# Kernel optimization log

Hardware: AMD Instinct MI355X
Metric: run time of the kernel (lower is better)

The kernel has to match this reference:

```python
import jax, jax.numpy as jnp
import numpy as np

K_NN = 20
EPS = 1e-5

def _conv1(x, w):
    # 1x1 Conv1d: w [O,C], x [B,C,N] -> [B,O,N]
    return jnp.einsum('oc,bcn->bon', w, x)

def _bn_eval(x, g, b):
    # BatchNorm1d in eval mode with running_mean=0, running_var=1
    return x * (g / np.sqrt(1.0 + EPS))[None, :, None] + b[None, :, None]

def _gn(x, g, b, groups=32):
    B, C, N = x.shape
    xr = x.reshape(B, groups, C // groups, N)
    mu = xr.mean(axis=(2, 3), keepdims=True)
    var = xr.var(axis=(2, 3), keepdims=True)
    xn = ((xr - mu) * jax.lax.rsqrt(var + EPS)).reshape(B, C, N)
    return xn * g[None, :, None] + b[None, :, None]

def _lrelu(x):
    return jnp.where(x >= 0, x, 0.2 * x)

def _graph_cross_attention(x, y, k):
    # x:[B,C,N] query features, y:[B,C,M] key features
    xn = x / jnp.linalg.norm(x, axis=1, keepdims=True)
    yn = y / jnp.linalg.norm(y, axis=1, keepdims=True)
    simi = jnp.einsum('bcn,bcm->bnm', xn, yn)          # cosine similarity [B,N,M]
    s, idx = jax.lax.top_k(simi, k)                    # [B,N,k] values and indices
    yt = jnp.swapaxes(y, 1, 2)                         # [B,M,C]
    nn = jax.vmap(lambda yb, ib: yb[ib])(yt, idx)      # gather neighbors [B,N,k,C]
    xt = jnp.swapaxes(x, 1, 2)                         # [B,N,C]
    diff = nn - xt[:, :, None, :]                      # edge features
    w = jax.nn.softmax(s, axis=-1)                     # attention over k neighbors
    agg = jnp.einsum('bnk,bnkc->bnc', w, diff)         # weighted aggregation
    return jnp.swapaxes(jnp.concatenate([xt, agg], axis=-1), 1, 2)  # [B,2C,N]

def setup_inputs() -> dict:
    key = jax.random.key(0)
    ks = jax.random.split(key, 22)
    B, N = 8, 2048
    f = lambda k, s: jax.random.normal(k, s, dtype=jnp.float32)
    return {
        'x1': f(ks[0], (B, 64, N)),
        'x2': f(ks[1], (B, 64, N)),
        'x3': f(ks[2], (B, 128, N)),
        'y3': f(ks[3], (B, 128, N)),
        'w4': f(ks[4], (256, 256)) * 0.06,
        'bn4_g': 1.0 + 0.1 * f(ks[5], (256,)),
        'bn4_b': 0.1 * f(ks[6], (256,)),
        'w5': f(ks[7], (512, 512)) * 0.04,
        'gn5_g': 1.0 + 0.1 * f(ks[8], (512,)),
        'gn5_b': 0.1 * f(ks[9], (512,)),
        'wm1': f(ks[10], (512, 512)) * 0.04,
        'bm1': 0.02 * f(ks[11], (512,)),
        'gn6_g': 1.0 + 0.1 * f(ks[12], (512,)),
        'gn6_b': 0.1 * f(ks[13], (512,)),
        'wm2': f(ks[14], (256, 512)) * 0.04,
        'bm2': 0.02 * f(ks[15], (256,)),
        'gn7_g': 1.0 + 0.1 * f(ks[16], (256,)),
        'gn7_b': 0.1 * f(ks[17], (256,)),
        'wm3': f(ks[18], (128, 256)) * 0.06,
        'bm3': 0.02 * f(ks[19], (128,)),
        'gn8_g': 1.0 + 0.1 * f(ks[20], (128,)),
        'gn8_b': 0.1 * f(ks[21], (128,)),
    }

def reference(x1, x2, x3, y3, w4, bn4_g, bn4_b, w5, gn5_g, gn5_b, wm1, bm1, gn6_g, gn6_b, wm2, bm2, gn7_g, gn7_b, wm3, bm3, gn8_g, gn8_b):
    x = _graph_cross_attention(x3, y3, K_NN)                  # [B,256,N]
    x4 = _lrelu(_bn_eval(_conv1(x, w4), bn4_g, bn4_b))        # conv4 [B,256,N]
    x = jnp.concatenate([x1, x2, x3, x4], axis=1)             # [B,512,N]
    local_concat = _lrelu(_gn(_conv1(x, w5), gn5_g, gn5_b))   # conv5 [B,512,N]
    gmax = local_concat.max(axis=2)
    gavg = local_concat.mean(axis=2)
    global_vector = jnp.concatenate([gmax, gavg], axis=1)     # [B,1024]
    h = jax.nn.relu(_gn(_conv1(local_concat, wm1) + bm1[None, :, None], gn6_g, gn6_b))
    h = jax.nn.relu(_gn(_conv1(h, wm2) + bm2[None, :, None], gn7_g, gn7_b))
    emb = jax.nn.relu(_gn(_conv1(h, wm3) + bm3[None, :, None], gn8_g, gn8_b))
    return emb, global_vector[:, :, None]
```

## Files before the change

kernel.cpp:

```cpp
#include <hip/hip_runtime.h>
#include <math.h>

#define N2 2048
#define LRELU_S 0.2f
#define BN4_RS 0.9999950000374997f

typedef short bf16x8 __attribute__((ext_vector_type(8)));
typedef float f32x16 __attribute__((ext_vector_type(16)));

__device__ __forceinline__ unsigned short bhi(float v) { return (unsigned short)(__float_as_uint(v) >> 16); }
__device__ __forceinline__ float bhif(float v) { return __uint_as_float(__float_as_uint(v) & 0xFFFF0000u); }
__device__ __forceinline__ float bf2f(unsigned short u) { return __uint_as_float(((unsigned int)u) << 16); }

__device__ __forceinline__ void gl16(const void* g, void* l) {
    __builtin_amdgcn_global_load_lds((const __attribute__((address_space(1))) unsigned int*)g,
                                     (__attribute__((address_space(3))) unsigned int*)l, 16, 0, 0);
}

__device__ __forceinline__ f32x16 z16() {
    f32x16 v;
    #pragma unroll
    for (int i = 0; i < 16; ++i) v[i] = 0.f;
    return v;
}

#define MFMA32 __builtin_amdgcn_mfma_f32_32x32x16_bf16

template<int ASRC, int EPI, int PASSES>
__global__ __launch_bounds__(256) void mgemm(
    const unsigned short* __restrict__ a1H, const unsigned short* __restrict__ a1L, int CA,
    const unsigned short* __restrict__ a2H, const unsigned short* __restrict__ a2L,
    const unsigned short* __restrict__ a3H, const unsigned short* __restrict__ a3L,
    const unsigned short* __restrict__ a4H, const unsigned short* __restrict__ a4L,
    const unsigned short* __restrict__ bH,  const unsigned short* __restrict__ bL, long bBs,
    int Ktot, int OC, int bbase,
    float* __restrict__ outF, unsigned short* __restrict__ oH,
    const float* __restrict__ epg, const float* __restrict__ epb,
    float* __restrict__ cs1, float* __restrict__ cs2)
{
    __shared__ alignas(16) unsigned short lAh[4096], lBh[4096];
    __shared__ alignas(16) unsigned short lAl[PASSES == 3 ? 4096 : 16];
    __shared__ alignas(16) unsigned short lBl[PASSES == 3 ? 4096 : 16];
    const int t  = threadIdx.x;
    const int n0 = blockIdx.x * 128;
    const int o0 = blockIdx.y * 128;
    const int bz = blockIdx.z;
    const int b  = bbase + bz;

    const int lane = t & 63;
    const int h    = lane >> 5;
    const int l31  = lane & 31;
    const int wid  = t >> 6;
    const int wm   = wid >> 1;
    const int wn   = wid & 1;
    const int sw   = (l31 >> 1) & 3;

    f32x16 acc00 = z16(), acc01 = z16(), acc10 = z16(), acc11 = z16();

    const int q0 = t, q1 = t + 256;
    const int r0 = q0 >> 2, p0 = q0 & 3, c0s = p0 ^ ((r0 >> 1) & 3);
    const int r1 = q1 >> 2, p1 = q1 & 3, c1s = p1 ^ ((r1 >> 1) & 3);

    const int rA0 = (wm * 64 + l31) * 32, rA1 = rA0 + 1024;
    const int rB0 = (wn * 64 + l31) * 32, rB1 = rB0 + 1024;

    for (int kc = 0; kc < Ktot; kc += 32) {
        const unsigned short *sAH, *sAL; int koff, Cs;
        if (ASRC == 0)      { sAH = a1H; sAL = a1L; koff = kc;       Cs = CA; }
        else if (ASRC == 1) {
            if (kc < 128)   { sAH = a1H; sAL = a1L; koff = kc;       Cs = 128; }
            else            { sAH = a2H; sAL = a2L; koff = kc - 128; Cs = 128; }
        } else {
            if (kc < 64)        { sAH = a1H; sAL = a1L; koff = kc;       Cs = 64;  }
            else if (kc < 128)  { sAH = a2H; sAL = a2L; koff = kc - 64;  Cs = 64;  }
            else if (kc < 256)  { sAH = a3H; sAL = a3L; koff = kc - 128; Cs = 128; }
            else                { sAH = a4H; sAL = a4L; koff = kc - 256; Cs = 256; }
        }
        __syncthreads();
        {
            long ga = ((long)b * N2 + n0 + r0) * Cs + koff + c0s * 8;
            long gb = (long)b * bBs + (long)(o0 + r0) * Ktot + kc + c0s * 8;
            gl16(sAH + ga, lAh + q0 * 8);
            gl16(bH + gb, lBh + q0 * 8);
            if (PASSES == 3) { gl16(sAL + ga, lAl + q0 * 8); gl16(bL + gb, lBl + q0 * 8); }
            long ga1 = ((long)b * N2 + n0 + r1) * Cs + koff + c1s * 8;
            long gb1 = (long)b * bBs + (long)(o0 + r1) * Ktot + kc + c1s * 8;
            gl16(sAH + ga1, lAh + q1 * 8);
            gl16(bH + gb1, lBh + q1 * 8);
            if (PASSES == 3) { gl16(sAL + ga1, lAl + q1 * 8); gl16(bL + gb1, lBl + q1 * 8); }
        }
        __syncthreads();
        #pragma unroll
        for (int s = 0; s < 2; ++s) {
            const int off = ((s * 2 + h) ^ sw) * 8;
            bf16x8 a0h = *(const bf16x8*)(lAh + rA0 + off);
            bf16x8 a1h_ = *(const bf16x8*)(lAh + rA1 + off);
            bf16x8 b0h = *(const bf16x8*)(lBh + rB0 + off);
            bf16x8 b1h = *(const bf16x8*)(lBh + rB1 + off);
            acc00 = MFMA32(a0h, b0h, acc00, 0, 0, 0);
            acc01 = MFMA32(a0h, b1h, acc01, 0, 0, 0);
            acc10 = MFMA32(a1h_, b0h, acc10, 0, 0, 0);
            acc11 = MFMA32(a1h_, b1h, acc11, 0, 0, 0);
            if (PASSES == 3) {
                bf16x8 a0l = *(const bf16x8*)(lAl + rA0 + off);
                bf16x8 a1l_ = *(const bf16x8*)(lAl + rA1 + off);
                bf16x8 b0l = *(const bf16x8*)(lBl + rB0 + off);
                bf16x8 b1l = *(const bf16x8*)(lBl + rB1 + off);
                acc00 = MFMA32(a0h, b0l, acc00, 0, 0, 0);
                acc00 = MFMA32(a0l, b0h, acc00, 0, 0, 0);
                acc01 = MFMA32(a0h, b1l, acc01, 0, 0, 0);
                acc01 = MFMA32(a0l, b1h, acc01, 0, 0, 0);
                acc10 = MFMA32(a1h_, b0l, acc10, 0, 0, 0);
                acc10 = MFMA32(a1l_, b0h, acc10, 0, 0, 0);
                acc11 = MFMA32(a1h_, b1l, acc11, 0, 0, 0);
                acc11 = MFMA32(a1l_, b1h, acc11, 0, 0, 0);
            }
        }
    }

    #pragma unroll
    for (int ni = 0; ni < 2; ++ni) {
        const int o = o0 + wn * 64 + ni * 32 + l31;
        float sc = 0.f, sh = 0.f, bias = 0.f;
        if (EPI == 1) { sc = epg[o] * BN4_RS; sh = epb[o]; }
        if (EPI == 2) { bias = epb ? epb[o] : 0.f; }
        float s1 = 0.f, s2 = 0.f;
        #pragma unroll
        for (int mi = 0; mi < 2; ++mi) {
            #pragma unroll
            for (int r = 0; r < 16; ++r) {
                const int n = n0 + wm * 64 + mi * 32 + (r & 3) + 8 * (r >> 2) + 4 * h;
                float v = (ni == 0) ? (mi == 0 ? acc00[r] : acc10[r])
                                    : (mi == 0 ? acc01[r] : acc11[r]);
                const long oi = ((long)bz * N2 + n) * (long)OC + o;
                if (EPI == 0) {
                    outF[oi] = v;
                } else if (EPI == 1) {
                    v = fmaf(v, sc, sh);
                    v = v >= 0.f ? v : LRELU_S * v;
                    oH[oi] = bhi(v);
                } else {
                    v += bias;
                    outF[oi] = v;
                    s1 += v; s2 = fmaf(v, v, s2);
                }
            }
        }
        if (EPI == 2) {
            s1 += __shfl_xor(s1, 32);
            s2 += __shfl_xor(s2, 32);
            if (h == 0) {
                atomicAdd(cs1 + bz * OC + o, s1);
                atomicAdd(cs2 + bz * OC + o, s2);
            }
        }
    }
}

__global__ void normK(const float* __restrict__ x3, const float* __restrict__ y3,
                      float* __restrict__ invnx, float* __restrict__ invny)
{
    const int n = blockIdx.x * 256 + threadIdx.x;
    const int b = blockIdx.y;
    const float* src = blockIdx.z ? y3 : x3;
    float ss = 0.f;
    for (int c = 0; c < 128; ++c) {
        float v = src[((long)b * 128 + c) * N2 + n];
        ss = fmaf(v, v, ss);
    }
    (blockIdx.z ? invny : invnx)[b * N2 + n] = rsqrtf(ss);
}

template<int MODE>
__global__ __launch_bounds__(256) void tsplitK(
    const float* __restrict__ in, int C,
    unsigned short* __restrict__ tHi, const float* __restrict__ invn,
    unsigned short* __restrict__ sHi, unsigned short* __restrict__ sLo,
    float* __restrict__ tF)
{
    __shared__ float lt[64 * 65];
    const int t = threadIdx.x;
    const int n0 = blockIdx.x * 64, c0 = blockIdx.y * 64, b = blockIdx.z;
    {
        const int nl = t & 63;
        const int cb = t >> 6;
        #pragma unroll
        for (int i = 0; i < 16; ++i) {
            const int cl = cb + 4 * i;
            lt[nl * 65 + cl] = in[((long)b * C + c0 + cl) * N2 + n0 + nl];
        }
    }
    __syncthreads();
    const int cl = t & 63;
    const int nb = t >> 6;
    #pragma unroll
    for (int i = 0; i < 16; ++i) {
        const int nl = nb + 4 * i;
        const float v = lt[nl * 65 + cl];
        const long oi = ((long)b * N2 + n0 + nl) * C + c0 + cl;
        if (MODE & 1) tHi[oi] = bhi(v);
        if (MODE & 2) {
            const float svv = v * invn[b * N2 + n0 + nl];
            sHi[oi] = bhi(svv); sLo[oi] = bhi(svv - bhif(svv));
        }
        if (MODE & 4) tF[oi] = v;
    }
}

__global__ void wsplitK(const float* __restrict__ w4, const float* __restrict__ w5,
    const float* __restrict__ wm1, const float* __restrict__ wm2, const float* __restrict__ wm3,
    unsigned short* __restrict__ w4h, unsigned short* __restrict__ w5h,
    unsigned short* __restrict__ m1h, unsigned short* __restrict__ m2h,
    unsigned short* __restrict__ m3h)
{
    const int y = blockIdx.y;
    const int idx = blockIdx.x * 256 + threadIdx.x;
    float v; unsigned short* dh;
    if (y == 0) {
        if (idx >= 256 * 256) return;
        const int k = idx & 255;
        v = w4[idx];
        if (k < 128) v -= w4[idx + 128];
        dh = w4h;
    } else if (y == 1) {
        if (idx >= 512 * 512) return;
        v = w5[idx]; dh = w5h;
    } else if (y == 2) {
        if (idx >= 512 * 512) return;
        v = wm1[idx]; dh = m1h;
    } else if (y == 3) {
        if (idx >= 256 * 512) return;
        v = wm2[idx]; dh = m2h;
    } else {
        if (idx >= 128 * 256) return;
        v = wm3[idx]; dh = m3h;
    }
    dh[idx] = bhi(v);
}

__global__ __launch_bounds__(256) void topkK(const float* __restrict__ simi,
    float* __restrict__ topw, int* __restrict__ topi, int bbase)
{
    __shared__ unsigned int hist[256];
    __shared__ unsigned int bcast[2];
    __shared__ unsigned int cnt[2];
    __shared__ float selv[20];
    __shared__ int   seli[20];
    const int t  = threadIdx.x;
    const int n  = blockIdx.x;
    const int bl = blockIdx.y;
    const float* row = simi + ((long)bl * N2 + n) * N2;

    float    f[8];
    unsigned u[8];
    {
        const float4 v0 = *(const float4*)(row + 4 * t);
        const float4 v1 = *(const float4*)(row + 1024 + 4 * t);
        f[0] = v0.x; f[1] = v0.y; f[2] = v0.z; f[3] = v0.w;
        f[4] = v1.x; f[5] = v1.y; f[6] = v1.z; f[7] = v1.w;
        #pragma unroll
        for (int i = 0; i < 8; ++i) {
            unsigned ub = __float_as_uint(f[i]);
            u[i] = ub ^ (((int)ub >> 31) | 0x80000000u);
        }
    }

    unsigned prefix = 0;
    unsigned kneed  = 20;
    #pragma unroll
    for (int pass = 0; pass < 4; ++pass) {
        const int shift = 24 - 8 * pass;
        const unsigned pmask = (pass == 0) ? 0u : (0xFFFFFFFFu << (shift + 8));
        hist[t] = 0;
        __syncthreads();
        #pragma unroll
        for (int i = 0; i < 8; ++i)
            if ((u[i] & pmask) == prefix)
                atomicAdd(&hist[(u[i] >> shift) & 255], 1u);
        __syncthreads();
        if (t < 64) {
            const unsigned h0 = hist[4 * t], h1 = hist[4 * t + 1];
            const unsigned h2 = hist[4 * t + 2], h3 = hist[4 * t + 3];
            const unsigned s3 = h3, s2 = h2 + s3, s1 = h1 + s2, s0 = h0 + s1;
            unsigned inc = s0;
            #pragma unroll
            for (int off = 1; off < 64; off <<= 1) {
                const unsigned o = __shfl_down(inc, off);
                if (t + off < 64) inc += o;
            }
            const unsigned excl = inc - s0;
            const unsigned sf[5] = {excl + s0, excl + s1, excl + s2, excl + s3, excl};
            #pragma unroll
            for (int j = 0; j < 4; ++j) {
                if (sf[j] >= kneed && sf[j + 1] < kneed) {
                    bcast[0] = 4 * t + j;
                    bcast[1] = kneed - sf[j + 1];
                }
            }
        }
        __syncthreads();
        prefix |= bcast[0] << shift;
        kneed   = bcast[1];
        __syncthreads();
    }

    if (t == 0) { cnt[0] = 0; cnt[1] = 0; }
    __syncthreads();
    const unsigned Tu = prefix;
    const int eqneed = (int)kneed;
    const int gt     = 20 - eqneed;
    #pragma unroll
    for (int i = 0; i < 8; ++i) {
        const int idx = (i < 4) ? (4 * t + i) : (1024 + 4 * t + (i - 4));
        if (u[i] > Tu) {
            const unsigned s = atomicAdd(&cnt[0], 1u);
            selv[s] = f[i]; seli[s] = idx;
        } else if (u[i] == Tu) {
            const unsigned e = atomicAdd(&cnt[1], 1u);
            if ((int)e < eqneed) { selv[gt + e] = f[i]; seli[gt + e] = idx; }
        }
    }
    __syncthreads();

    if (t < 64) {
        const float v = (t < 20) ? selv[t] : -1e30f;
        float m = v;
        #pragma unroll
        for (int off = 1; off < 32; off <<= 1) m = fmaxf(m, __shfl_xor(m, off, 32));
        const float e = (t < 20) ? expf(v - m) : 0.f;
        float s = e;
        #pragma unroll
        for (int off = 1; off < 32; off <<= 1) s += __shfl_xor(s, off, 32);
        if (t < 20) {
            const long base = (((long)(bbase + bl)) * N2 + n) * 20;
            topw[base + t] = e / s;
            topi[base + t] = seli[t];
        }
    }
}

__global__ __launch_bounds__(256) void aggK(const float* __restrict__ yT,
    const float* __restrict__ topw, const int* __restrict__ topi,
    unsigned short* __restrict__ Gh)
{
    const int t  = threadIdx.x;
    const int c4 = (t & 31) * 4;
    const int ns = t >> 5;
    const int b  = blockIdx.x;
    const int n  = blockIdx.y * 8 + ns;
    const long tb = ((long)b * N2 + n) * 20;
    const float* yb = yT + (long)b * N2 * 128 + c4;

    float a0 = 0.f, a1 = 0.f, a2 = 0.f, a3 = 0.f;
    #pragma unroll
    for (int k = 0; k < 20; ++k) {
        const float w  = topw[tb + k];
        const int  idx = topi[tb + k];
        const float4 v = *(const float4*)(yb + (long)idx * 128);
        a0 = fmaf(w, v.x, a0);
        a1 = fmaf(w, v.y, a1);
        a2 = fmaf(w, v.z, a2);
        a3 = fmaf(w, v.w, a3);
    }
    const long oi = ((long)b * N2 + n) * 128 + c4;
    ushort4 hh;
    hh.x = bhi(a0); hh.y = bhi(a1); hh.z = bhi(a2); hh.w = bhi(a3);
    *(ushort4*)(Gh + oi) = hh;
}

__global__ void statsK(const float* __restrict__ cs1, const float* __restrict__ cs2,
    float* __restrict__ stats, int C)
{
    const int t = threadIdx.x;
    const int b = t >> 5, g = t & 31;
    const int cpg = C >> 5;
    float s1 = 0.f, s2 = 0.f;
    for (int j = 0; j < cpg; ++j) {
        s1 += cs1[b * C + g * cpg + j];
        s2 += cs2[b * C + g * cpg + j];
    }
    const float cnt = (float)(cpg * N2);
    const float mu = s1 / cnt;
    const float var = s2 / cnt - mu * mu;
    stats[t * 2] = mu;
    stats[t * 2 + 1] = rsqrtf(var + 1e-5f);
}

template<int ACT, int LC>
__global__ void gnapplyK(const float* __restrict__ pre, const float* __restrict__ stats,
    const float* __restrict__ gamma, const float* __restrict__ beta,
    unsigned short* __restrict__ oH)
{
    const long i4 = ((long)blockIdx.x * 256 + threadIdx.x) * 4;
    const int C = 1 << LC;
    const int c = (int)(i4 & (C - 1));
    const int bn = (int)(i4 >> LC);
    const int b = bn >> 11;
    const int g = c >> (LC - 5);
    const float mu = stats[(b * 32 + g) * 2];
    const float rs = stats[(b * 32 + g) * 2 + 1];
    const float4 gm = *(const float4*)(gamma + c);
    const float4 bt = *(const float4*)(beta + c);
    const float4 v = *(const float4*)(pre + i4);
    const float vals[4] = {v.x, v.y, v.z, v.w};
    const float gms[4] = {gm.x, gm.y, gm.z, gm.w};
    const float bts[4] = {bt.x, bt.y, bt.z, bt.w};
    unsigned short hs[4];
    #pragma unroll
    for (int j = 0; j < 4; ++j) {
        float x = (vals[j] - mu) * (rs * gms[j]) + bts[j];
        x = (ACT == 0) ? (x >= 0.f ? x : LRELU_S * x) : (x >= 0.f ? x : 0.f);
        hs[j] = bhi(x);
    }
    ushort4 hh; hh.x = hs[0]; hh.y = hs[1]; hh.z = hs[2]; hh.w = hs[3];
    *(ushort4*)(oH + i4) = hh;
}

__global__ __launch_bounds__(256) void gnfinalK(const float* __restrict__ pre,
    const float* __restrict__ stats, const float* __restrict__ gamma,
    const float* __restrict__ beta, float* __restrict__ out)
{
    __shared__ float lt[64 * 65];
    const int t = threadIdx.x;
    const int n0 = blockIdx.x * 64, c0 = blockIdx.y * 64, b = blockIdx.z;
    {
        const int cl = t & 63;
        const int nb = t >> 6;
        const int c = c0 + cl;
        const int g = c >> 2;
        const float mu = stats[(b * 32 + g) * 2];
        const float rs = stats[(b * 32 + g) * 2 + 1];
        const float sc = rs * gamma[c], sh = beta[c] - mu * sc;
        #pragma unroll
        for (int i = 0; i < 16; ++i) {
            const int nl = nb + 4 * i;
            float v = pre[((long)b * N2 + n0 + nl) * 128 + c];
            v = v * sc + sh;
            lt[cl * 65 + nl] = v > 0.f ? v : 0.f;
        }
    }
    __syncthreads();
    const int nl = t & 63;
    const int cb = t >> 6;
    #pragma unroll
    for (int i = 0; i < 16; ++i) {
        const int cl = cb + 4 * i;
        out[((long)b * 128 + c0 + cl) * N2 + n0 + nl] = lt[cl * 65 + nl];
    }
}

__global__ __launch_bounds__(256) void pool1K(const unsigned short* __restrict__ lcH,
    float* __restrict__ pmax, float* __restrict__ psum)
{
    __shared__ float lmx[512], lsm[512];
    const int t  = threadIdx.x;
    const int cq = t & 127;
    const int rp = t >> 7;
    const int nch = blockIdx.x;
    const int b   = blockIdx.y;
    float mx[4] = {-1e30f, -1e30f, -1e30f, -1e30f};
    float sm[4] = {0.f, 0.f, 0.f, 0.f};
    for (int i = 0; i < 32; ++i) {
        const int n = nch * 64 + 2 * i + rp;
        const long base = ((long)b * N2 + n) * 512 + cq * 4;
        const ushort4 hh = *(const ushort4*)(lcH + base);
        const float v0 = bf2f(hh.x);
        const float v1 = bf2f(hh.y);
        const float v2 = bf2f(hh.z);
        const float v3 = bf2f(hh.w);
        mx[0] = fmaxf(mx[0], v0); sm[0] += v0;
        mx[1] = fmaxf(mx[1], v1); sm[1] += v1;
        mx[2] = fmaxf(mx[2], v2); sm[2] += v2;
        mx[3] = fmaxf(mx[3], v3); sm[3] += v3;
    }
    if (rp) {
        #pragma unroll
        for (int j = 0; j < 4; ++j) { lmx[cq * 4 + j] = mx[j]; lsm[cq * 4 + j] = sm[j]; }
    }
    __syncthreads();
    if (!rp) {
        const long pb = ((long)(b * 32 + nch)) * 512 + cq * 4;
        #pragma unroll
        for (int j = 0; j < 4; ++j) {
            pmax[pb + j] = fmaxf(mx[j], lmx[cq * 4 + j]);
            psum[pb + j] = sm[j] + lsm[cq * 4 + j];
        }
    }
}

__global__ void pool2K(const float* __restrict__ pmax, const float* __restrict__ psum,
                       float* __restrict__ gv)
{
    const int t = threadIdx.x;
    const int b = blockIdx.x;
    float mx0 = -1e30f, mx1 = -1e30f, s0 = 0.f, s1 = 0.f;
    for (int nch = 0; nch < 32; ++nch) {
        const long pb = ((long)(b * 32 + nch)) * 512 + 2 * t;
        const float2 pm = *(const float2*)(pmax + pb);
        const float2 ps = *(const float2*)(psum + pb);
        mx0 = fmaxf(mx0, pm.x); mx1 = fmaxf(mx1, pm.y);
        s0 += ps.x; s1 += ps.y;
    }
    gv[b * 1024 + 2 * t]           = mx0;
    gv[b * 1024 + 2 * t + 1]       = mx1;
    gv[b * 1024 + 512 + 2 * t]     = s0 * (1.f / 2048.f);
    gv[b * 1024 + 512 + 2 * t + 1] = s1 * (1.f / 2048.f);
}

extern "C" void kernel_launch(void* const* d_in, const int* in_sizes, int n_in,
                              void* d_out, int out_size, void* d_ws, size_t ws_size,
                              hipStream_t stream)
{
    const float* x1    = (const float*)d_in[0];
    const float* x2    = (const float*)d_in[1];
    const float* x3    = (const float*)d_in[2];
    const float* y3    = (const float*)d_in[3];
    const float* w4    = (const float*)d_in[4];
    const float* bn4g  = (const float*)d_in[5];
    const float* bn4b  = (const float*)d_in[6];
    const float* w5    = (const float*)d_in[7];
    const float* gn5g  = (const float*)d_in[8];
    const float* gn5b  = (const float*)d_in[9];
    const float* wm1   = (const float*)d_in[10];
    const float* bm1   = (const float*)d_in[11];
    const float* gn6g  = (const float*)d_in[12];
    const float* gn6b  = (const float*)d_in[13];
    const float* wm2   = (const float*)d_in[14];
    const float* bm2   = (const float*)d_in[15];
    const float* gn7g  = (const float*)d_in[16];
    const float* gn7b  = (const float*)d_in[17];
    const float* wm3   = (const float*)d_in[18];
    const float* bm3   = (const float*)d_in[19];
    const float* gn8g  = (const float*)d_in[20];
    const float* gn8b  = (const float*)d_in[21];
    float* out = (float*)d_out;
    (void)in_sizes; (void)n_in; (void)out_size; (void)ws_size;

    char* ws = (char*)d_ws;
    float*          simiF = (float*)(ws + 0);
    float*          bufPS = (float*)(ws + 0);
    unsigned short* lcH   = (unsigned short*)(ws + 134217728);
    unsigned short* h1H   = (unsigned short*)(ws + 150994944);
    unsigned short* x4H   = (unsigned short*)(ws + 167772160);
    unsigned short* h2H   = (unsigned short*)(ws + 176160768);
    float*          yT    = (float*)(ws + 184549376);
    unsigned short* x3tH  = (unsigned short*)(ws + 192937984);
    unsigned short* GH    = (unsigned short*)(ws + 197132288);
    unsigned short* xnH   = (unsigned short*)(ws + 201326592);
    unsigned short* xnL   = (unsigned short*)(ws + 205520896);
    unsigned short* ynH   = (unsigned short*)(ws + 209715200);
    unsigned short* ynL   = (unsigned short*)(ws + 213909504);
    unsigned short* x1tH  = (unsigned short*)(ws + 218103808);
    unsigned short* x2tH  = (unsigned short*)(ws + 220200960);
    unsigned short* w4pH  = (unsigned short*)(ws + 222298112);
    unsigned short* w5H   = (unsigned short*)(ws + 222429184);
    unsigned short* m1H   = (unsigned short*)(ws + 222953472);
    unsigned short* m2H   = (unsigned short*)(ws + 223477760);
    unsigned short* m3H   = (unsigned short*)(ws + 223739904);
    float* invnx = (float*)(ws + 223805440);
    float* invny = (float*)(ws + 223870976);
    float* topw  = (float*)(ws + 223936512);
    int*   topi  = (int*)  (ws + 225247232);
    float* csb   = (float*)(ws + 226557952);
    float* cs1_5 = csb,          *cs2_5 = csb + 4096;
    float* cs1_6 = csb + 8192,   *cs2_6 = csb + 12288;
    float* cs1_7 = csb + 16384,  *cs2_7 = csb + 20480;
    float* cs1_8 = csb + 24576,  *cs2_8 = csb + 28672;
    float* stats5 = (float*)(ws + 226689024);
    float* stats6 = stats5 + 512;
    float* stats7 = stats5 + 1024;
    float* stats8 = stats5 + 1536;
    float* pmax  = (float*)(ws + 226697216);
    float* psum  = (float*)(ws + 227221504);

    const dim3 B256(256);
    const unsigned short* nu = nullptr;

    hipMemsetAsync(csb, 0, 131072, stream);

    normK<<<dim3(8, 8, 2), B256, 0, stream>>>(x3, y3, invnx, invny);
    tsplitK<6><<<dim3(32, 2, 8), B256, 0, stream>>>(y3, 128, nullptr, invny, ynH, ynL, yT);
    tsplitK<3><<<dim3(32, 2, 8), B256, 0, stream>>>(x3, 128, x3tH, invnx, xnH, xnL, nullptr);
    tsplitK<1><<<dim3(32, 1, 8), B256, 0, stream>>>(x1, 64, x1tH, nullptr, nullptr, nullptr, nullptr);
    tsplitK<1><<<dim3(32, 1, 8), B256, 0, stream>>>(x2, 64, x2tH, nullptr, nullptr, nullptr, nullptr);
    wsplitK<<<dim3(1024, 5), B256, 0, stream>>>(w4, w5, wm1, wm2, wm3,
        w4pH, w5H, m1H, m2H, m3H);

    mgemm<0, 0, 3><<<dim3(16, 16, 8), B256, 0, stream>>>(
        xnH, xnL, 128, nu, nu, nu, nu, nu, nu,
        ynH, ynL, (long)N2 * 128, 128, 2048, 0,
        simiF, nullptr, nullptr, nullptr, nullptr, nullptr);
    topkK<<<dim3(2048, 8), B256, 0, stream>>>(simiF, topw, topi, 0);

    aggK<<<dim3(8, 256), B256, 0, stream>>>(yT, topw, topi, GH);

    mgemm<1, 1, 1><<<dim3(16, 2, 8), B256, 0, stream>>>(
        x3tH, nu, 128, GH, nu, nu, nu, nu, nu,
        w4pH, nu, 0, 256, 256, 0,
        nullptr, x4H, bn4g, bn4b, nullptr, nullptr);

    mgemm<2, 2, 1><<<dim3(16, 4, 8), B256, 0, stream>>>(
        x1tH, nu, 64, x2tH, nu, x3tH, nu, x4H, nu,
        w5H, nu, 0, 512, 512, 0,
        bufPS, nullptr, nullptr, nullptr, cs1_5, cs2_5);
    statsK<<<1, B256, 0, stream>>>(cs1_5, cs2_5, stats5, 512);
    gnapplyK<0, 9><<<8192, B256, 0, stream>>>(bufPS, stats5, gn5g, gn5b, lcH);

    pool1K<<<dim3(32, 8), B256, 0, stream>>>(lcH, pmax, psum);
    pool2K<<<dim3(8), B256, 0, stream>>>(pmax, psum, out + (long)8 * 128 * 2048);

    mgemm<0, 2, 1><<<dim3(16, 4, 8), B256, 0, stream>>>(
        lcH, nu, 512, nu, nu, nu, nu, nu, nu,
        m1H, nu, 0, 512, 512, 0,
        bufPS, nullptr, nullptr, bm1, cs1_6, cs2_6);
    statsK<<<1, B256, 0, stream>>>(cs1_6, cs2_6, stats6, 512);
    gnapplyK<1, 9><<<8192, B256, 0, stream>>>(bufPS, stats6, gn6g, gn6b, h1H);

    mgemm<0, 2, 1><<<dim3(16, 2, 8), B256, 0, stream>>>(
        h1H, nu, 512, nu, nu, nu, nu, nu, nu,
        m2H, nu, 0, 512, 256, 0,
        bufPS, nullptr, nullptr, bm2, cs1_7, cs2_7);
    statsK<<<1, B256, 0, stream>>>(cs1_7, cs2_7, stats7, 256);
    gnapplyK<1, 8><<<4096, B256, 0, stream>>>(bufPS, stats7, gn7g, gn7b, h2H);

    mgemm<0, 2, 1><<<dim3(16, 1, 8), B256, 0, stream>>>(
        h2H, nu, 256, nu, nu, nu, nu, nu, nu,
        m3H, nu, 0, 256, 128, 0,
        bufPS, nullptr, nullptr, bm3, cs1_8, cs2_8);
    statsK<<<1, B256, 0, stream>>>(cs1_8, cs2_8, stats8, 128);
    gnfinalK<<<dim3(32, 2, 8), B256, 0, stream>>>(bufPS, stats8, gn8g, gn8b, out);
}
```

Measured before the change: 389.5 us.

## Replace 4-pass radix top-k select with min/max binned histogram plus candidate ranking

The per-row top-20 selection no longer runs four 8-bit radix histogram passes. It now computes the row min and max, quantizes values into 256 linear bins, and finds the threshold bin with one histogram pass. Candidates in the threshold bin are ranked exactly by pairwise comparison when there are at most 256 of them, which removes several barrier-heavy passes. If more than 256 candidates land in that bin, the fallback takes them in arbitrary atomic order, so the selected set can differ from exact top-k.

```diff
diff --git a/kernel.cpp b/kernel.cpp
--- a/kernel.cpp
+++ b/kernel.cpp
@@ -243,7 +243,11 @@
 {
     __shared__ unsigned int hist[256];
     __shared__ unsigned int bcast[2];
-    __shared__ unsigned int cnt[2];
+    __shared__ float lmn[4], lmx[4];
+    __shared__ unsigned int cnt0, candCnt, tick;
+    __shared__ unsigned int candU[256];
+    __shared__ float candV[256];
+    __shared__ int   candI[256];
     __shared__ float selv[20];
     __shared__ int   seli[20];
     const int t  = threadIdx.x;
@@ -265,59 +269,89 @@
         }
     }
 
-    unsigned prefix = 0;
-    unsigned kneed  = 20;
-    #pragma unroll
-    for (int pass = 0; pass < 4; ++pass) {
-        const int shift = 24 - 8 * pass;
-        const unsigned pmask = (pass == 0) ? 0u : (0xFFFFFFFFu << (shift + 8));
-        hist[t] = 0;
-        __syncthreads();
-        #pragma unroll
-        for (int i = 0; i < 8; ++i)
-            if ((u[i] & pmask) == prefix)
-                atomicAdd(&hist[(u[i] >> shift) & 255], 1u);
-        __syncthreads();
-        if (t < 64) {
-            const unsigned h0 = hist[4 * t], h1 = hist[4 * t + 1];
-            const unsigned h2 = hist[4 * t + 2], h3 = hist[4 * t + 3];
-            const unsigned s3 = h3, s2 = h2 + s3, s1 = h1 + s2, s0 = h0 + s1;
-            unsigned inc = s0;
-            #pragma unroll
-            for (int off = 1; off < 64; off <<= 1) {
-                const unsigned o = __shfl_down(inc, off);
-                if (t + off < 64) inc += o;
+    float tmn = f[0], tmx = f[0];
+    #pragma unroll
+    for (int i = 1; i < 8; ++i) { tmn = fminf(tmn, f[i]); tmx = fmaxf(tmx, f[i]); }
+    #pragma unroll
+    for (int off = 1; off < 64; off <<= 1) {
+        tmn = fminf(tmn, __shfl_xor(tmn, off));
+        tmx = fmaxf(tmx, __shfl_xor(tmx, off));
+    }
+    if ((t & 63) == 0) { lmn[t >> 6] = tmn; lmx[t >> 6] = tmx; }
+    if (t == 0) { cnt0 = 0; candCnt = 0; tick = 0; }
+    hist[t] = 0;
+    __syncthreads();
+    const float rmn = fminf(fminf(lmn[0], lmn[1]), fminf(lmn[2], lmn[3]));
+    const float rmx = fmaxf(fmaxf(lmx[0], lmx[1]), fmaxf(lmx[2], lmx[3]));
+    const float rng = rmx - rmn;
+    const float scale = (rng > 0.f) ? (255.0f / rng) : 0.f;
+
+    int q[8];
+    #pragma unroll
+    for (int i = 0; i < 8; ++i) {
+        int qi = (int)((f[i] - rmn) * scale);
+        q[i] = qi < 0 ? 0 : (qi > 255 ? 255 : qi);
+        atomicAdd(&hist[q[i]], 1u);
+    }
+    __syncthreads();
+
+    if (t < 64) {
+        const unsigned h0 = hist[4 * t], h1 = hist[4 * t + 1];
+        const unsigned h2 = hist[4 * t + 2], h3 = hist[4 * t + 3];
+        const unsigned s3 = h3, s2 = h2 + s3, s1 = h1 + s2, s0 = h0 + s1;
+        unsigned inc = s0;
+        #pragma unroll
+        for (int off = 1; off < 64; off <<= 1) {
+            const unsigned o = __shfl_down(inc, off);
+            if (t + off < 64) inc += o;
+        }
+        const unsigned excl = inc - s0;
+        const unsigned sf[5] = {excl + s0, excl + s1, excl + s2, excl + s3, excl};
+        #pragma unroll
+        for (int j = 0; j < 4; ++j) {
+            if (sf[j] >= 20u && sf[j + 1] < 20u) {
+                bcast[0] = 4 * t + j;
+                bcast[1] = 20u - sf[j + 1];
             }
-            const unsigned excl = inc - s0;
-            const unsigned sf[5] = {excl + s0, excl + s1, excl + s2, excl + s3, excl};
-            #pragma unroll
-            for (int j = 0; j < 4; ++j) {
-                if (sf[j] >= kneed && sf[j + 1] < kneed) {
-                    bcast[0] = 4 * t + j;
-                    bcast[1] = kneed - sf[j + 1];
-                }
-            }
-        }
-        __syncthreads();
-        prefix |= bcast[0] << shift;
-        kneed   = bcast[1];
-        __syncthreads();
-    }
-
-    if (t == 0) { cnt[0] = 0; cnt[1] = 0; }
-    __syncthreads();
-    const unsigned Tu = prefix;
-    const int eqneed = (int)kneed;
-    const int gt     = 20 - eqneed;
+        }
+    }
+    __syncthreads();
+    const int Abin   = (int)bcast[0];
+    const int kneedA = (int)bcast[1];
+    const int gt     = 20 - kneedA;
+
     #pragma unroll
     for (int i = 0; i < 8; ++i) {
         const int idx = (i < 4) ? (4 * t + i) : (1024 + 4 * t + (i - 4));
-        if (u[i] > Tu) {
-            const unsigned s = atomicAdd(&cnt[0], 1u);
+        if (q[i] > Abin) {
+            const unsigned s = atomicAdd(&cnt0, 1u);
             selv[s] = f[i]; seli[s] = idx;
-        } else if (u[i] == Tu) {
-            const unsigned e = atomicAdd(&cnt[1], 1u);
-            if ((int)e < eqneed) { selv[gt + e] = f[i]; seli[gt + e] = idx; }
+        } else if (q[i] == Abin) {
+            const unsigned s = atomicAdd(&candCnt, 1u);
+            if (s < 256u) { candU[s] = u[i]; candV[s] = f[i]; candI[s] = idx; }
+        }
+    }
+    __syncthreads();
+
+    const int cc = (int)candCnt;
+    if (cc <= 256) {
+        for (int slot = t; slot < cc; slot += 256) {
+            const unsigned ui = candU[slot];
+            int r = 0;
+            for (int j = 0; j < cc; ++j) {
+                const unsigned uj = candU[j];
+                r += (uj > ui) || (uj == ui && j < slot);
+            }
+            if (r < kneedA) { selv[gt + r] = candV[slot]; seli[gt + r] = candI[slot]; }
+        }
+    } else {
+        #pragma unroll
+        for (int i = 0; i < 8; ++i) {
+            const int idx = (i < 4) ? (4 * t + i) : (1024 + 4 * t + (i - 4));
+            if (q[i] == Abin) {
+                const unsigned e = atomicAdd(&tick, 1u);
+                if ((int)e < kneedA) { selv[gt + e] = f[i]; seli[gt + e] = idx; }
+            }
         }
     }
     __syncthreads();
```

Result: faster. 358.2 us (-8.0%).
